# Kernel optimization log

Hardware: AMD Instinct MI355X
Metric: run time of the kernel (lower is better)

## Reference

```python
import jax, jax.numpy as jnp
import numpy as np
from jax import lax

K = 5  # SCNN_KERNEL_LENGTH
PAD = K - 1
PAD_L = PAD // 2
PAD_R = PAD - PAD_L


def setup_inputs() -> dict:
    key = jax.random.key(0)
    k1, k2 = jax.random.split(key)
    B, H, W, C = 16, 256, 256, 32
    inputs = jax.random.normal(k1, (B, H, W, C), dtype=jnp.float32)
    # keras 'random_uniform' init is small; scale randn similarly to keep relu chain stable
    w = jax.random.normal(k2, (C, K, 1, C), dtype=jnp.float32) * 0.05
    b = jnp.zeros((C,), dtype=jnp.float32)
    return {"inputs": inputs, "w": w, "b": b}


def _mvcnn_down(inputs, w, b):
    # inputs: [B,H,W,C]; w: [C,K,1,C] (tf filter: [fh=C, fw=K, in=1, out=C])
    # The tf conv of the transposed row [B,C,W,1] with this filter is exactly a
    # 1D conv over W mixing all C input channels:
    #   out[b,x,o] = sum_{k,c} row_pad[b, x+k, c] * w[c,k,0,o]
    kernel = jnp.transpose(w[:, :, 0, :], (1, 0, 2))  # [K, C_in, C_out]

    def conv_row(x):  # x: [B,W,C] -> [B,W,C]
        return lax.conv_general_dilated(
            x, kernel, window_strides=(1,), padding=[(PAD_L, PAD_R)],
            dimension_numbers=("NWC", "WIO", "NWC"))

    rows = jnp.transpose(inputs, (1, 0, 2, 3))  # [H,B,W,C]

    def step(carry, row):
        # row i of the evolving state = original row + relu-conv result of row i-1
        x = row + carry
        r = jax.nn.relu(conv_row(x) + b)
        return r, r

    init = jnp.zeros_like(rows[0])
    _, out_rows = lax.scan(step, init, rows)  # [H,B,W,C]
    return jnp.transpose(out_rows, (1, 0, 2, 3))  # [B,H,W,C]


def reference(inputs, w, b):
    return _mvcnn_down(inputs, w, b)
```

## Files before the change

### kernel.cpp

```cpp
#include <hip/hip_runtime.h>
#include <stdint.h>

typedef _Float16 f16;
typedef _Float16 f16x2 __attribute__((ext_vector_type(2)));
typedef _Float16 f16x8 __attribute__((ext_vector_type(8)));
typedef float f32x4 __attribute__((ext_vector_type(4)));

#define NB 16
#define NH 256
#define NW 256
#define NC 32
#define NK 5

#define OWN 8
#define GC 32
#define NBLK (NB * GC)
#define XSTR 40
#define XROWS 44

#define FLAG_U32 16
#define NFLAGS (NBLK * 2 * FLAG_U32)
#define MAIL_BASE NFLAGS
#define MAIL_WORDS 128
#define KEYOF(k) (0x5EED0000u ^ (uint32_t)(k))

__device__ __forceinline__ void lds_barrier() {
  asm volatile("s_waitcnt lgkmcnt(0)\n\ts_barrier" ::: "memory");
}

__global__ __launch_bounds__(192, 2)
void mvcnn_down_mb(const float* __restrict__ in, const float* __restrict__ wt,
                   const float* __restrict__ bias, float* __restrict__ out,
                   uint32_t* __restrict__ ws) {
  __shared__ __align__(16) f16 xpad[2][XROWS * XSTR];

  const int bid  = blockIdx.x;
  const int b    = bid & 15;
  const int ck   = bid >> 4;
  const int t    = threadIdx.x;
  const int lane = t & 63;
  const int wv   = t >> 6;
  const int n16  = lane & 15;
  const int q    = lane >> 4;

  const int TB = (wv == 0) ? 0 : (wv == 1 ? 16 : 24);

  f16x8 bfrag[NK][2];
  #pragma unroll
  for (int tap = 0; tap < NK; ++tap) {
    #pragma unroll
    for (int nt = 0; nt < 2; ++nt) {
      f16x8 f;
      #pragma unroll
      for (int j = 0; j < 8; ++j) {
        int cch = q * 4 + (j >> 1) + (j & 1) * 16;
        f[j] = (f16)wt[(cch * NK + tap) * NC + nt * 16 + n16];
      }
      bfrag[tap][nt] = f;
    }
  }
  const float bias0 = bias[n16];
  const float bias1 = bias[16 + n16];

  for (int i = t; i < 2 * XROWS * XSTR; i += 192) (&xpad[0][0])[i] = (f16)0.f;
  __syncthreads();

  const float* inb  = in  + (size_t)b * NH * NW * NC;
  float*       outb = out + (size_t)b * NH * NW * NC;

  const int cl0 = TB + q * 4;
  const int g0  = ck * OWN - 16 + cl0;
  const int arow = TB + n16;

  uint32_t* flags = ws;
  uint32_t* mail  = ws + MAIL_BASE;

  const int  rsrc   = (wv == 0) ? (q < 2 ? ck - 2 : ck - 1)
                                : (q < 2 ? ck + 1 : ck + 2);
  const bool rvalid = (wv != 1) && ((unsigned)rsrc < GC);
  const int  rmidx  = ((q & 1) * 4) * 16 + n16;
  const int  smidx  = (q * 4) * 16 + n16;

  float pf0[8], pf1[8];
  auto load_row = [&](int h1, float (&pf)[8]) {
    if (h1 >= NH) return;
    const float* rp = inb + (size_t)h1 * NW * NC;
    #pragma unroll
    for (int r = 0; r < 4; ++r) {
      int g  = g0 + r;
      int gc = g < 0 ? 0 : (g > NW - 1 ? NW - 1 : g);
      pf[2 * r]     = rp[gc * NC + n16];
      pf[2 * r + 1] = rp[gc * NC + 16 + n16];
    }
  };

  #pragma unroll
  for (int r = 0; r < 4; ++r) {
    int g = g0 + r;
    if ((unsigned)g < NW) {
      f16x2 v;
      v[0] = (f16)inb[g * NC + n16];
      v[1] = (f16)inb[g * NC + 16 + n16];
      *(f16x2*)(&xpad[0][(cl0 + r + 2) * XSTR + 2 * n16]) = v;
    }
  }
  load_row(1, pf0);
  load_row(2, pf1);
  __syncthreads();

  auto body = [&](const int h, float (&pf)[8], f16* xc, f16* xn) {
    if (h > 0 && (h & 7) == 0) {
      const int k  = h >> 3;
      const int ms = k & 1;
      if (wv != 1) {
        if (lane < 2) {
          int sc = (wv == 0) ? (ck - 1 - lane) : (ck + 1 + lane);
          if ((unsigned)sc < GC) {
            const int sbid = sc * 16 + b;
            while (__hip_atomic_load(&flags[(sbid * 2 + ms) * FLAG_U32],
                                     __ATOMIC_RELAXED, __HIP_MEMORY_SCOPE_AGENT)
                   != KEYOF(k))
              __builtin_amdgcn_s_sleep(2);
          }
        }
        asm volatile("" ::: "memory");
        if (rvalid) {
          const uint32_t* mb =
              mail + ((size_t)(rsrc * 16 + b) * 2 + ms) * MAIL_WORDS;
          #pragma unroll
          for (int r = 0; r < 4; ++r) {
            uint32_t u = __hip_atomic_load(&mb[rmidx + r * 16],
                                           __ATOMIC_RELAXED,
                                           __HIP_MEMORY_SCOPE_AGENT);
            *(uint32_t*)(&xc[(cl0 + r + 2) * XSTR + 2 * n16]) = u;
          }
        }
      }
      lds_barrier();
    }

    f32x4 acc0 = {bias0, bias0, bias0, bias0};
    f32x4 acc1 = {bias1, bias1, bias1, bias1};
    #pragma unroll
    for (int tap = 0; tap < NK; ++tap) {
      f16x8 af = *(const f16x8*)(xc + (arow + tap) * XSTR + q * 8);
      acc0 = __builtin_amdgcn_mfma_f32_16x16x32_f16(af, bfrag[tap][0], acc0, 0, 0, 0);
      acc1 = __builtin_amdgcn_mfma_f32_16x16x32_f16(af, bfrag[tap][1], acc1, 0, 0, 0);
    }

    uint32_t sb[4] = {0, 0, 0, 0};
    float y0v[4], y1v[4];
    #pragma unroll
    for (int r = 0; r < 4; ++r) {
      float y0 = fmaxf(acc0[r], 0.f);
      float y1 = fmaxf(acc1[r], 0.f);
      y0v[r] = y0; y1v[r] = y1;
      int g = g0 + r;
      if (h < NH - 1 && (unsigned)g < NW) {
        f16x2 v;
        v[0] = (f16)(pf[2 * r]     + y0);
        v[1] = (f16)(pf[2 * r + 1] + y1);
        *(f16x2*)(&xn[(cl0 + r + 2) * XSTR + 2 * n16]) = v;
        sb[r] = __builtin_bit_cast(uint32_t, v);
      }
    }

    const bool sendrow = (((h + 1) & 7) == 0) && (h + 1 < NH);
    if (sendrow && wv == 1) {
      const int k  = (h + 1) >> 3;
      const int ms = k & 1;
      if (q < 2) {
        uint32_t* mb = mail + ((size_t)bid * 2 + ms) * MAIL_WORDS;
        #pragma unroll
        for (int r = 0; r < 4; ++r)
          __hip_atomic_store(&mb[smidx + r * 16], sb[r],
                             __ATOMIC_RELAXED, __HIP_MEMORY_SCOPE_AGENT);
      }
      asm volatile("s_waitcnt vmcnt(0)" ::: "memory");
      if (lane == 0)
        __hip_atomic_store(&flags[(bid * 2 + ms) * FLAG_U32], KEYOF(k),
                           __ATOMIC_RELAXED, __HIP_MEMORY_SCOPE_AGENT);
    }

    if (wv == 1 && q < 2) {
      float* orow = outb + (size_t)h * NW * NC;
      #pragma unroll
      for (int r = 0; r < 4; ++r) {
        const int g = g0 + r;
        orow[g * NC + n16]      = y0v[r];
        orow[g * NC + 16 + n16] = y1v[r];
      }
    }

    load_row(h + 3, pf);
    lds_barrier();
  };

  for (int h = 0; h < NH; h += 2) {
    body(h,     pf0, &xpad[0][0], &xpad[1][0]);
    body(h + 1, pf1, &xpad[1][0], &xpad[0][0]);
  }
}

__global__ __launch_bounds__(1024, 4)
void mvcnn_down(const float* __restrict__ in, const float* __restrict__ wt,
                const float* __restrict__ bias, float* __restrict__ out) {
  __shared__ __align__(16) f16 xpad[2][260 * XSTR];

  const int b    = blockIdx.x;
  const int t    = threadIdx.x;
  const int lane = t & 63;
  const int wv   = t >> 6;
  const int n16  = lane & 15;
  const int q    = lane >> 4;

  f16x8 bfrag[NK][2];
  #pragma unroll
  for (int tap = 0; tap < NK; ++tap) {
    #pragma unroll
    for (int nt = 0; nt < 2; ++nt) {
      f16x8 f;
      #pragma unroll
      for (int j = 0; j < 8; ++j) {
        int cch = q * 4 + (j >> 1) + (j & 1) * 16;
        f[j] = (f16)wt[(cch * NK + tap) * NC + nt * 16 + n16];
      }
      bfrag[tap][nt] = f;
    }
  }
  const float bias0 = bias[n16];
  const float bias1 = bias[16 + n16];

  for (int i = t; i < 2 * 260 * XSTR; i += 1024) (&xpad[0][0])[i] = (f16)0.f;
  __syncthreads();

  const float* inb  = in  + (size_t)b * NH * NW * NC;
  float*       outb = out + (size_t)b * NH * NW * NC;

  const int wo0  = wv * 16 + q * 4;
  const int arow = wv * 16 + n16;

  float pf0[8], pf1[8];
  auto load_in_row = [&](int h1, float (&pf)[8]) {
    const float* rp = inb + (size_t)h1 * NW * NC;
    #pragma unroll
    for (int r = 0; r < 4; ++r) {
      int wo = wo0 + r;
      pf[2 * r]     = rp[wo * NC + n16];
      pf[2 * r + 1] = rp[wo * NC + 16 + n16];
    }
  };

  #pragma unroll
  for (int r = 0; r < 4; ++r) {
    int wo = wo0 + r;
    f16x2 v;
    v[0] = (f16)inb[wo * NC + n16];
    v[1] = (f16)inb[wo * NC + 16 + n16];
    *(f16x2*)(&xpad[0][(wo + 2) * XSTR + 2 * n16]) = v;
  }
  load_in_row(1, pf0);
  load_in_row(2, pf1);
  __syncthreads();

  auto body = [&](const int h, float (&pf)[8], const f16* xp_cur, f16* xp_nxt) {
    f32x4 acc0 = {0.f, 0.f, 0.f, 0.f};
    f32x4 acc1 = {0.f, 0.f, 0.f, 0.f};
    #pragma unroll
    for (int tap = 0; tap < NK; ++tap) {
      f16x8 af = *(const f16x8*)(xp_cur + (arow + tap) * XSTR + q * 8);
      acc0 = __builtin_amdgcn_mfma_f32_16x16x32_f16(af, bfrag[tap][0], acc0, 0, 0, 0);
      acc1 = __builtin_amdgcn_mfma_f32_16x16x32_f16(af, bfrag[tap][1], acc1, 0, 0, 0);
    }
    float* orow = outb + (size_t)h * NW * NC;
    #pragma unroll
    for (int r = 0; r < 4; ++r) {
      float y0 = acc0[r] + bias0; y0 = y0 > 0.f ? y0 : 0.f;
      float y1 = acc1[r] + bias1; y1 = y1 > 0.f ? y1 : 0.f;
      int wo = wo0 + r;
      orow[wo * NC + n16]      = y0;
      orow[wo * NC + 16 + n16] = y1;
      if (h < NH - 1) {
        f16x2 v;
        v[0] = (f16)(pf[2 * r]     + y0);
        v[1] = (f16)(pf[2 * r + 1] + y1);
        *(f16x2*)(&xp_nxt[(wo + 2) * XSTR + 2 * n16]) = v;
      }
    }
    if (h + 3 < NH) load_in_row(h + 3, pf);
    lds_barrier();
  };

  const f16* xA = &xpad[0][0];
  f16* xB = &xpad[1][0];
  for (int h = 0; h < NH; h += 2) {
    body(h,     pf0, xA, xB);
    body(h + 1, pf1, xB, (f16*)xA);
  }
}

extern "C" void kernel_launch(void* const* d_in, const int* in_sizes, int n_in,
                              void* d_out, int out_size, void* d_ws, size_t ws_size,
                              hipStream_t stream) {
  const float* in   = (const float*)d_in[0];
  const float* wt   = (const float*)d_in[1];
  const float* bias = (const float*)d_in[2];
  float* out = (float*)d_out;

  const size_t need = (size_t)(NFLAGS + NBLK * 2 * MAIL_WORDS) * 4;
  if (d_ws != nullptr && ws_size >= need) {
    hipLaunchKernelGGL(mvcnn_down_mb, dim3(NBLK), dim3(192), 0, stream,
                       in, wt, bias, out, (uint32_t*)d_ws);
  } else {
    hipLaunchKernelGGL(mvcnn_down, dim3(NB), dim3(1024), 0, stream,
                       in, wt, bias, out);
  }
}
```

Baseline: 418.4 us.

## Collapse halo-exchange block to one wavefront owning 16 columns, drop barriers

```diff
diff --git a/kernel.cpp b/kernel.cpp
--- a/kernel.cpp
+++ b/kernel.cpp
@@ -12,23 +12,23 @@
 #define NC 32
 #define NK 5
 
-#define OWN 8
-#define GC 32
+#define OWN 16
+#define GC 16
 #define NBLK (NB * GC)
 #define XSTR 40
-#define XROWS 44
+#define XROWS 52
 
 #define FLAG_U32 16
 #define NFLAGS (NBLK * 2 * FLAG_U32)
 #define MAIL_BASE NFLAGS
-#define MAIL_WORDS 128
+#define MAIL_WORDS 256
 #define KEYOF(k) (0x5EED0000u ^ (uint32_t)(k))
 
 __device__ __forceinline__ void lds_barrier() {
   asm volatile("s_waitcnt lgkmcnt(0)\n\ts_barrier" ::: "memory");
 }
 
-__global__ __launch_bounds__(192, 2)
+__global__ __launch_bounds__(64, 1)
 void mvcnn_down_mb(const float* __restrict__ in, const float* __restrict__ wt,
                    const float* __restrict__ bias, float* __restrict__ out,
                    uint32_t* __restrict__ ws) {
@@ -37,13 +37,9 @@
   const int bid  = blockIdx.x;
   const int b    = bid & 15;
   const int ck   = bid >> 4;
-  const int t    = threadIdx.x;
-  const int lane = t & 63;
-  const int wv   = t >> 6;
+  const int lane = threadIdx.x;
   const int n16  = lane & 15;
   const int q    = lane >> 4;
-
-  const int TB = (wv == 0) ? 0 : (wv == 1 ? 16 : 24);
 
   f16x8 bfrag[NK][2];
   #pragma unroll
@@ -62,143 +58,158 @@
   const float bias0 = bias[n16];
   const float bias1 = bias[16 + n16];
 
-  for (int i = t; i < 2 * XROWS * XSTR; i += 192) (&xpad[0][0])[i] = (f16)0.f;
-  __syncthreads();
+  for (int i = lane; i < (int)(2 * XROWS * XSTR / 2); i += 64)
+    ((uint32_t*)&xpad[0][0])[i] = 0u;
 
   const float* inb  = in  + (size_t)b * NH * NW * NC;
   float*       outb = out + (size_t)b * NH * NW * NC;
 
-  const int cl0 = TB + q * 4;
-  const int g0  = ck * OWN - 16 + cl0;
-  const int arow = TB + n16;
-
   uint32_t* flags = ws;
   uint32_t* mail  = ws + MAIL_BASE;
 
-  const int  rsrc   = (wv == 0) ? (q < 2 ? ck - 2 : ck - 1)
-                                : (q < 2 ? ck + 1 : ck + 2);
-  const bool rvalid = (wv != 1) && ((unsigned)rsrc < GC);
-  const int  rmidx  = ((q & 1) * 4) * 16 + n16;
-  const int  smidx  = (q * 4) * 16 + n16;
-
-  float pf0[8], pf1[8];
-  auto load_row = [&](int h1, float (&pf)[8]) {
+  const int gbase = ck * OWN - 16;
+
+  float pf0[24], pf1[24];
+  auto load_row = [&](int h1, float (&pf)[24]) {
     if (h1 >= NH) return;
     const float* rp = inb + (size_t)h1 * NW * NC;
     #pragma unroll
+    for (int tl = 0; tl < 3; ++tl) {
+      #pragma unroll
+      for (int r = 0; r < 4; ++r) {
+        int g  = gbase + tl * 16 + q * 4 + r;
+        int gc = g < 0 ? 0 : (g > NW - 1 ? NW - 1 : g);
+        pf[(tl * 4 + r) * 2]     = rp[gc * NC + n16];
+        pf[(tl * 4 + r) * 2 + 1] = rp[gc * NC + 16 + n16];
+      }
+    }
+  };
+
+  #pragma unroll
+  for (int tl = 0; tl < 3; ++tl) {
+    #pragma unroll
     for (int r = 0; r < 4; ++r) {
-      int g  = g0 + r;
-      int gc = g < 0 ? 0 : (g > NW - 1 ? NW - 1 : g);
-      pf[2 * r]     = rp[gc * NC + n16];
-      pf[2 * r + 1] = rp[gc * NC + 16 + n16];
-    }
-  };
-
-  #pragma unroll
-  for (int r = 0; r < 4; ++r) {
-    int g = g0 + r;
-    if ((unsigned)g < NW) {
-      f16x2 v;
-      v[0] = (f16)inb[g * NC + n16];
-      v[1] = (f16)inb[g * NC + 16 + n16];
-      *(f16x2*)(&xpad[0][(cl0 + r + 2) * XSTR + 2 * n16]) = v;
+      int lc = tl * 16 + q * 4 + r;
+      int g  = gbase + lc;
+      if ((unsigned)g < NW) {
+        f16x2 v;
+        v[0] = (f16)inb[g * NC + n16];
+        v[1] = (f16)inb[g * NC + 16 + n16];
+        *(f16x2*)(&xpad[0][(lc + 2) * XSTR + 2 * n16]) = v;
+      }
     }
   }
   load_row(1, pf0);
   load_row(2, pf1);
-  __syncthreads();
-
-  auto body = [&](const int h, float (&pf)[8], f16* xc, f16* xn) {
+
+  auto body = [&](const int h, float (&pf)[24], f16* xc, f16* xn) {
     if (h > 0 && (h & 7) == 0) {
       const int k  = h >> 3;
       const int ms = k & 1;
-      if (wv != 1) {
-        if (lane < 2) {
-          int sc = (wv == 0) ? (ck - 1 - lane) : (ck + 1 + lane);
-          if ((unsigned)sc < GC) {
-            const int sbid = sc * 16 + b;
-            while (__hip_atomic_load(&flags[(sbid * 2 + ms) * FLAG_U32],
-                                     __ATOMIC_RELAXED, __HIP_MEMORY_SCOPE_AGENT)
-                   != KEYOF(k))
-              __builtin_amdgcn_s_sleep(2);
-          }
+      if (lane < 2) {
+        const bool have = lane ? (ck < GC - 1) : (ck > 0);
+        if (have) {
+          const int nbid = bid + (lane ? 16 : -16);
+          while (__hip_atomic_load(&flags[(nbid * 2 + ms) * FLAG_U32],
+                                   __ATOMIC_RELAXED, __HIP_MEMORY_SCOPE_AGENT)
+                 != KEYOF(k))
+            __builtin_amdgcn_s_sleep(2);
         }
-        asm volatile("" ::: "memory");
-        if (rvalid) {
-          const uint32_t* mb =
-              mail + ((size_t)(rsrc * 16 + b) * 2 + ms) * MAIL_WORDS;
-          #pragma unroll
-          for (int r = 0; r < 4; ++r) {
-            uint32_t u = __hip_atomic_load(&mb[rmidx + r * 16],
-                                           __ATOMIC_RELAXED,
-                                           __HIP_MEMORY_SCOPE_AGENT);
-            *(uint32_t*)(&xc[(cl0 + r + 2) * XSTR + 2 * n16]) = u;
-          }
+      }
+      asm volatile("" ::: "memory");
+      if (ck > 0) {
+        const uint32_t* mb = mail + ((size_t)(bid - 16) * 2 + ms) * MAIL_WORDS;
+        #pragma unroll
+        for (int r = 0; r < 4; ++r) {
+          uint32_t u = __hip_atomic_load(&mb[(q * 4 + r) * 16 + n16],
+                                         __ATOMIC_RELAXED,
+                                         __HIP_MEMORY_SCOPE_AGENT);
+          *(uint32_t*)(&xc[(q * 4 + r + 2) * XSTR + 2 * n16]) = u;
         }
       }
-      lds_barrier();
-    }
-
-    f32x4 acc0 = {bias0, bias0, bias0, bias0};
-    f32x4 acc1 = {bias1, bias1, bias1, bias1};
-    #pragma unroll
-    for (int tap = 0; tap < NK; ++tap) {
-      f16x8 af = *(const f16x8*)(xc + (arow + tap) * XSTR + q * 8);
-      acc0 = __builtin_amdgcn_mfma_f32_16x16x32_f16(af, bfrag[tap][0], acc0, 0, 0, 0);
-      acc1 = __builtin_amdgcn_mfma_f32_16x16x32_f16(af, bfrag[tap][1], acc1, 0, 0, 0);
+      if (ck < GC - 1) {
+        const uint32_t* mb = mail + ((size_t)(bid + 16) * 2 + ms) * MAIL_WORDS;
+        #pragma unroll
+        for (int r = 0; r < 4; ++r) {
+          uint32_t u = __hip_atomic_load(&mb[(q * 4 + r) * 16 + n16],
+                                         __ATOMIC_RELAXED,
+                                         __HIP_MEMORY_SCOPE_AGENT);
+          *(uint32_t*)(&xc[(32 + q * 4 + r + 2) * XSTR + 2 * n16]) = u;
+        }
+      }
+    }
+
+    f32x4 acc[3][2];
+    #pragma unroll
+    for (int tl = 0; tl < 3; ++tl) {
+      acc[tl][0] = {bias0, bias0, bias0, bias0};
+      acc[tl][1] = {bias1, bias1, bias1, bias1};
+    }
+    #pragma unroll
+    for (int tl = 0; tl < 3; ++tl) {
+      #pragma unroll
+      for (int tap = 0; tap < NK; ++tap) {
+        f16x8 af = *(const f16x8*)(xc + (tl * 16 + n16 + tap) * XSTR + q * 8);
+        acc[tl][0] = __builtin_amdgcn_mfma_f32_16x16x32_f16(af, bfrag[tap][0],
+                                                            acc[tl][0], 0, 0, 0);
+        acc[tl][1] = __builtin_amdgcn_mfma_f32_16x16x32_f16(af, bfrag[tap][1],
+                                                            acc[tl][1], 0, 0, 0);
+      }
     }
 
     uint32_t sb[4] = {0, 0, 0, 0};
-    float y0v[4], y1v[4];
-    #pragma unroll
-    for (int r = 0; r < 4; ++r) {
-      float y0 = fmaxf(acc0[r], 0.f);
-      float y1 = fmaxf(acc1[r], 0.f);
-      y0v[r] = y0; y1v[r] = y1;
-      int g = g0 + r;
-      if (h < NH - 1 && (unsigned)g < NW) {
-        f16x2 v;
-        v[0] = (f16)(pf[2 * r]     + y0);
-        v[1] = (f16)(pf[2 * r + 1] + y1);
-        *(f16x2*)(&xn[(cl0 + r + 2) * XSTR + 2 * n16]) = v;
-        sb[r] = __builtin_bit_cast(uint32_t, v);
-      }
-    }
-
-    const bool sendrow = (((h + 1) & 7) == 0) && (h + 1 < NH);
-    if (sendrow && wv == 1) {
+    float y0m[4], y1m[4];
+    #pragma unroll
+    for (int tl = 0; tl < 3; ++tl) {
+      #pragma unroll
+      for (int r = 0; r < 4; ++r) {
+        float y0 = fmaxf(acc[tl][0][r], 0.f);
+        float y1 = fmaxf(acc[tl][1][r], 0.f);
+        const int lc = tl * 16 + q * 4 + r;
+        const int g  = gbase + lc;
+        if (tl == 1) { y0m[r] = y0; y1m[r] = y1; }
+        if (h < NH - 1 && (unsigned)g < NW) {
+          f16x2 v;
+          v[0] = (f16)(pf[(tl * 4 + r) * 2]     + y0);
+          v[1] = (f16)(pf[(tl * 4 + r) * 2 + 1] + y1);
+          *(f16x2*)(&xn[(lc + 2) * XSTR + 2 * n16]) = v;
+          if (tl == 1) sb[r] = __builtin_bit_cast(uint32_t, v);
+        }
+      }
+    }
+
+    if (((h + 1) & 7) == 0 && (h + 1) < NH) {
       const int k  = (h + 1) >> 3;
       const int ms = k & 1;
-      if (q < 2) {
-        uint32_t* mb = mail + ((size_t)bid * 2 + ms) * MAIL_WORDS;
-        #pragma unroll
-        for (int r = 0; r < 4; ++r)
-          __hip_atomic_store(&mb[smidx + r * 16], sb[r],
-                             __ATOMIC_RELAXED, __HIP_MEMORY_SCOPE_AGENT);
-      }
+      uint32_t* mb = mail + ((size_t)bid * 2 + ms) * MAIL_WORDS;
+      #pragma unroll
+      for (int r = 0; r < 4; ++r)
+        __hip_atomic_store(&mb[(q * 4 + r) * 16 + n16], sb[r],
+                           __ATOMIC_RELAXED, __HIP_MEMORY_SCOPE_AGENT);
       asm volatile("s_waitcnt vmcnt(0)" ::: "memory");
       if (lane == 0)
         __hip_atomic_store(&flags[(bid * 2 + ms) * FLAG_U32], KEYOF(k),
                            __ATOMIC_RELAXED, __HIP_MEMORY_SCOPE_AGENT);
     }
 
-    if (wv == 1 && q < 2) {
+    {
       float* orow = outb + (size_t)h * NW * NC;
       #pragma unroll
       for (int r = 0; r < 4; ++r) {
-        const int g = g0 + r;
-        orow[g * NC + n16]      = y0v[r];
-        orow[g * NC + 16 + n16] = y1v[r];
+        const int g = ck * OWN + q * 4 + r;
+        orow[g * NC + n16]      = y0m[r];
+        orow[g * NC + 16 + n16] = y1m[r];
       }
     }
 
     load_row(h + 3, pf);
-    lds_barrier();
   };
 
+  f16* B0 = &xpad[0][0];
+  f16* B1 = &xpad[1][0];
   for (int h = 0; h < NH; h += 2) {
-    body(h,     pf0, &xpad[0][0], &xpad[1][0]);
-    body(h + 1, pf1, &xpad[1][0], &xpad[0][0]);
+    body(h,     pf0, B0, B1);
+    body(h + 1, pf1, B1, B0);
   }
 }
 
@@ -309,7 +320,7 @@
 
   const size_t need = (size_t)(NFLAGS + NBLK * 2 * MAIL_WORDS) * 4;
   if (d_ws != nullptr && ws_size >= need) {
-    hipLaunchKernelGGL(mvcnn_down_mb, dim3(NBLK), dim3(192), 0, stream,
+    hipLaunchKernelGGL(mvcnn_down_mb, dim3(NBLK), dim3(64), 0, stream,
                        in, wt, bias, out, (uint32_t*)d_ws);
   } else {
     hipLaunchKernelGGL(mvcnn_down, dim3(NB), dim3(1024), 0, stream,
```

After: 469.8 us. +12.3%, slower.

## Repartition column chunks to 16-wide with 2 waves and 4-row halo exchange

Applied to the files above, without the earlier changes.

```diff
diff --git a/kernel.cpp b/kernel.cpp
--- a/kernel.cpp
+++ b/kernel.cpp
@@ -12,14 +12,15 @@
 #define NC 32
 #define NK 5
 
-#define OWN 8
-#define GC 32
+#define OWN 16
+#define GC 16
 #define NBLK (NB * GC)
 #define XSTR 40
-#define XROWS 44
+#define XROWS 36
 
 #define FLAG_U32 16
-#define NFLAGS (NBLK * 2 * FLAG_U32)
+#define NSLOT (NBLK * 2 * 2)
+#define NFLAGS (NSLOT * FLAG_U32)
 #define MAIL_BASE NFLAGS
 #define MAIL_WORDS 128
 #define KEYOF(k) (0x5EED0000u ^ (uint32_t)(k))
@@ -28,7 +29,7 @@
   asm volatile("s_waitcnt lgkmcnt(0)\n\ts_barrier" ::: "memory");
 }
 
-__global__ __launch_bounds__(192, 2)
+__global__ __launch_bounds__(128, 1)
 void mvcnn_down_mb(const float* __restrict__ in, const float* __restrict__ wt,
                    const float* __restrict__ bias, float* __restrict__ out,
                    uint32_t* __restrict__ ws) {
@@ -43,8 +44,6 @@
   const int n16  = lane & 15;
   const int q    = lane >> 4;
 
-  const int TB = (wv == 0) ? 0 : (wv == 1 ? 16 : 24);
-
   f16x8 bfrag[NK][2];
   #pragma unroll
   for (int tap = 0; tap < NK; ++tap) {
@@ -62,88 +61,89 @@
   const float bias0 = bias[n16];
   const float bias1 = bias[16 + n16];
 
-  for (int i = t; i < 2 * XROWS * XSTR; i += 192) (&xpad[0][0])[i] = (f16)0.f;
-  __syncthreads();
+  for (int i = t; i < (int)(2 * XROWS * XSTR / 2); i += 128)
+    ((uint32_t*)&xpad[0][0])[i] = 0u;
 
   const float* inb  = in  + (size_t)b * NH * NW * NC;
   float*       outb = out + (size_t)b * NH * NW * NC;
 
-  const int cl0 = TB + q * 4;
-  const int g0  = ck * OWN - 16 + cl0;
-  const int arow = TB + n16;
+  const int lc0   = wv * 16 + q * 4;
+  const int gcol0 = ck * 16 - 8 + lc0;
+
+  int boff[4];
+  #pragma unroll
+  for (int r = 0; r < 4; ++r) {
+    int g  = gcol0 + r;
+    int gc = g < 0 ? 0 : (g > NW - 1 ? NW - 1 : g);
+    boff[r] = (gc * NC + n16) * 4;
+  }
+  const bool ostore = wv ? (q < 2) : (q >= 2);
+  const int  gown0  = wv ? (ck * 16 + 8 + q * 4) : (ck * 16 + (q - 2) * 4);
 
   uint32_t* flags = ws;
   uint32_t* mail  = ws + MAIL_BASE;
-
-  const int  rsrc   = (wv == 0) ? (q < 2 ? ck - 2 : ck - 1)
-                                : (q < 2 ? ck + 1 : ck + 2);
-  const bool rvalid = (wv != 1) && ((unsigned)rsrc < GC);
-  const int  rmidx  = ((q & 1) * 4) * 16 + n16;
-  const int  smidx  = (q * 4) * 16 + n16;
+  const bool haspeer = wv ? (ck < GC - 1) : (ck > 0);
+  const int  myslot2 = (bid * 2 + wv) * 2;
+  const int  nbslot2 = wv ? ((bid + 16) * 2 + 0) * 2
+                          : ((bid - 16) * 2 + 1) * 2;
+  const int  smi     = wv ? (q * 4) * 16 : ((q - 2) * 4) * 16;
 
   float pf0[8], pf1[8];
   auto load_row = [&](int h1, float (&pf)[8]) {
     if (h1 >= NH) return;
-    const float* rp = inb + (size_t)h1 * NW * NC;
+    const char* rp = (const char*)(inb + (size_t)h1 * NW * NC);
     #pragma unroll
     for (int r = 0; r < 4; ++r) {
-      int g  = g0 + r;
-      int gc = g < 0 ? 0 : (g > NW - 1 ? NW - 1 : g);
-      pf[2 * r]     = rp[gc * NC + n16];
-      pf[2 * r + 1] = rp[gc * NC + 16 + n16];
+      pf[2 * r]     = *(const float*)(rp + boff[r]);
+      pf[2 * r + 1] = *(const float*)(rp + boff[r] + 64);
     }
   };
 
   #pragma unroll
   for (int r = 0; r < 4; ++r) {
-    int g = g0 + r;
+    int g = gcol0 + r;
     if ((unsigned)g < NW) {
       f16x2 v;
       v[0] = (f16)inb[g * NC + n16];
       v[1] = (f16)inb[g * NC + 16 + n16];
-      *(f16x2*)(&xpad[0][(cl0 + r + 2) * XSTR + 2 * n16]) = v;
+      *(f16x2*)(&xpad[0][(lc0 + r + 2) * XSTR + 2 * n16]) = v;
     }
   }
   load_row(1, pf0);
   load_row(2, pf1);
   __syncthreads();
 
-  auto body = [&](const int h, float (&pf)[8], f16* xc, f16* xn) {
-    if (h > 0 && (h & 7) == 0) {
-      const int k  = h >> 3;
-      const int ms = k & 1;
-      if (wv != 1) {
-        if (lane < 2) {
-          int sc = (wv == 0) ? (ck - 1 - lane) : (ck + 1 + lane);
-          if ((unsigned)sc < GC) {
-            const int sbid = sc * 16 + b;
-            while (__hip_atomic_load(&flags[(sbid * 2 + ms) * FLAG_U32],
-                                     __ATOMIC_RELAXED, __HIP_MEMORY_SCOPE_AGENT)
-                   != KEYOF(k))
-              __builtin_amdgcn_s_sleep(2);
+  auto body = [&](const int h, float (&pf)[8], f16* xc, f16* xn,
+                  bool recv, bool send) {
+    if (recv) {
+      const int k = h >> 2, ms = k & 1;
+      if (haspeer) {
+        if (lane == 0) {
+          while (__hip_atomic_load(&flags[(nbslot2 + ms) * FLAG_U32],
+                                   __ATOMIC_RELAXED, __HIP_MEMORY_SCOPE_AGENT)
+                 != KEYOF(k))
+            __builtin_amdgcn_s_sleep(2);
+        }
+        asm volatile("" ::: "memory");
+        if (q < 2) {
+          const uint32_t* mb = mail + (size_t)(nbslot2 + ms) * MAIL_WORDS;
+          #pragma unroll
+          for (int r = 0; r < 4; ++r) {
+            uint32_t u = __hip_atomic_load(&mb[(q * 4 + r) * 16 + n16],
+                                           __ATOMIC_RELAXED,
+                                           __HIP_MEMORY_SCOPE_AGENT);
+            const int lc = (wv ? 24 : 0) + q * 4 + r;
+            *(uint32_t*)(&xc[(lc + 2) * XSTR + 2 * n16]) = u;
           }
         }
-        asm volatile("" ::: "memory");
-        if (rvalid) {
-          const uint32_t* mb =
-              mail + ((size_t)(rsrc * 16 + b) * 2 + ms) * MAIL_WORDS;
-          #pragma unroll
-          for (int r = 0; r < 4; ++r) {
-            uint32_t u = __hip_atomic_load(&mb[rmidx + r * 16],
-                                           __ATOMIC_RELAXED,
-                                           __HIP_MEMORY_SCOPE_AGENT);
-            *(uint32_t*)(&xc[(cl0 + r + 2) * XSTR + 2 * n16]) = u;
-          }
-        }
-      }
-      lds_barrier();
+      }
     }
 
     f32x4 acc0 = {bias0, bias0, bias0, bias0};
     f32x4 acc1 = {bias1, bias1, bias1, bias1};
     #pragma unroll
     for (int tap = 0; tap < NK; ++tap) {
-      f16x8 af = *(const f16x8*)(xc + (arow + tap) * XSTR + q * 8);
+      f16x8 af = *(const f16x8*)(xc + (wv * 16 + n16 + tap) * XSTR + q * 8);
       acc0 = __builtin_amdgcn_mfma_f32_16x16x32_f16(af, bfrag[tap][0], acc0, 0, 0, 0);
       acc1 = __builtin_amdgcn_mfma_f32_16x16x32_f16(af, bfrag[tap][1], acc1, 0, 0, 0);
     }
@@ -155,40 +155,39 @@
       float y0 = fmaxf(acc0[r], 0.f);
       float y1 = fmaxf(acc1[r], 0.f);
       y0v[r] = y0; y1v[r] = y1;
-      int g = g0 + r;
+      int g = gcol0 + r;
       if (h < NH - 1 && (unsigned)g < NW) {
         f16x2 v;
         v[0] = (f16)(pf[2 * r]     + y0);
         v[1] = (f16)(pf[2 * r + 1] + y1);
-        *(f16x2*)(&xn[(cl0 + r + 2) * XSTR + 2 * n16]) = v;
+        *(f16x2*)(&xn[(lc0 + r + 2) * XSTR + 2 * n16]) = v;
         sb[r] = __builtin_bit_cast(uint32_t, v);
       }
     }
 
-    const bool sendrow = (((h + 1) & 7) == 0) && (h + 1 < NH);
-    if (sendrow && wv == 1) {
-      const int k  = (h + 1) >> 3;
-      const int ms = k & 1;
-      if (q < 2) {
-        uint32_t* mb = mail + ((size_t)bid * 2 + ms) * MAIL_WORDS;
-        #pragma unroll
-        for (int r = 0; r < 4; ++r)
-          __hip_atomic_store(&mb[smidx + r * 16], sb[r],
+    if (send && (h + 1) < NH) {
+      const int k = (h + 1) >> 2, ms = k & 1;
+      if (haspeer) {
+        if (ostore) {
+          uint32_t* mb = mail + (size_t)(myslot2 + ms) * MAIL_WORDS;
+          #pragma unroll
+          for (int r = 0; r < 4; ++r)
+            __hip_atomic_store(&mb[smi + r * 16 + n16], sb[r],
+                               __ATOMIC_RELAXED, __HIP_MEMORY_SCOPE_AGENT);
+        }
+        asm volatile("s_waitcnt vmcnt(0)" ::: "memory");
+        if (lane == 0)
+          __hip_atomic_store(&flags[(myslot2 + ms) * FLAG_U32], KEYOF(k),
                              __ATOMIC_RELAXED, __HIP_MEMORY_SCOPE_AGENT);
       }
-      asm volatile("s_waitcnt vmcnt(0)" ::: "memory");
-      if (lane == 0)
-        __hip_atomic_store(&flags[(bid * 2 + ms) * FLAG_U32], KEYOF(k),
-                           __ATOMIC_RELAXED, __HIP_MEMORY_SCOPE_AGENT);
-    }
-
-    if (wv == 1 && q < 2) {
+    }
+
+    if (ostore) {
       float* orow = outb + (size_t)h * NW * NC;
       #pragma unroll
       for (int r = 0; r < 4; ++r) {
-        const int g = g0 + r;
-        orow[g * NC + n16]      = y0v[r];
-        orow[g * NC + 16 + n16] = y1v[r];
+        orow[(gown0 + r) * NC + n16]      = y0v[r];
+        orow[(gown0 + r) * NC + 16 + n16] = y1v[r];
       }
     }
 
@@ -196,9 +195,13 @@
     lds_barrier();
   };
 
-  for (int h = 0; h < NH; h += 2) {
-    body(h,     pf0, &xpad[0][0], &xpad[1][0]);
-    body(h + 1, pf1, &xpad[1][0], &xpad[0][0]);
+  f16* B0 = &xpad[0][0];
+  f16* B1 = &xpad[1][0];
+  for (int h4 = 0; h4 < NH; h4 += 4) {
+    body(h4,     pf0, B0, B1, h4 > 0, false);
+    body(h4 + 1, pf1, B1, B0, false,  false);
+    body(h4 + 2, pf0, B0, B1, false,  false);
+    body(h4 + 3, pf1, B1, B0, false,  true);
   }
 }
 
@@ -307,9 +310,9 @@
   const float* bias = (const float*)d_in[2];
   float* out = (float*)d_out;
 
-  const size_t need = (size_t)(NFLAGS + NBLK * 2 * MAIL_WORDS) * 4;
+  const size_t need = (size_t)(NFLAGS + NSLOT * MAIL_WORDS) * 4;
   if (d_ws != nullptr && ws_size >= need) {
-    hipLaunchKernelGGL(mvcnn_down_mb, dim3(NBLK), dim3(192), 0, stream,
+    hipLaunchKernelGGL(mvcnn_down_mb, dim3(NBLK), dim3(128), 0, stream,
                        in, wt, bias, out, (uint32_t*)d_ws);
   } else {
     hipLaunchKernelGGL(mvcnn_down, dim3(NB), dim3(1024), 0, stream,
```

Result: slower. 428.5 us (+2.4%).
